# Optimization experiments

Hardware: AMD Instinct MI355X
Metric: run time of the kernel (lower is better)

The kernel has to match this reference:

```python
import jax, jax.numpy as jnp
import numpy as np

N_HEADS = 16
D_MODEL = 1024
HEAD_DIM = D_MODEL // N_HEADS
B, S = 2, 2048


def setup_inputs() -> dict:
    key = jax.random.key(0)
    ks = jax.random.split(key, 10)
    scale = 1.0 / np.sqrt(D_MODEL)
    inp = {
        "query_tokens": jax.random.normal(ks[0], (B, S, D_MODEL), dtype=jnp.float32),
        "key_or_value_tokens": jax.random.normal(ks[1], (B, S, D_MODEL), dtype=jnp.float32),
        "mask": jnp.ones((B, S, S), dtype=jnp.int32),
        "Wq": jax.random.normal(ks[2], (D_MODEL, D_MODEL), dtype=jnp.float32) * scale,
        "bq": jnp.zeros((D_MODEL,), dtype=jnp.float32),
        "Wk": jax.random.normal(ks[3], (D_MODEL, D_MODEL), dtype=jnp.float32) * scale,
        "bk": jnp.zeros((D_MODEL,), dtype=jnp.float32),
        "Wv": jax.random.normal(ks[4], (D_MODEL, D_MODEL), dtype=jnp.float32) * scale,
        "bv": jnp.zeros((D_MODEL,), dtype=jnp.float32),
        "Wo": jax.random.normal(ks[5], (D_MODEL, D_MODEL), dtype=jnp.float32) * scale,
        "bo": jnp.zeros((D_MODEL,), dtype=jnp.float32),
    }
    return inp


def reference(query_tokens, key_or_value_tokens, mask, Wq, bq, Wk, bk, Wv, bv, Wo, bo):
    b, s, d = query_tokens.shape
    h, dh = N_HEADS, HEAD_DIM

    def proj(x, W, bias):
        # torch Linear: x @ W.T + b ; then split heads -> (b, h, s, dh)
        y = jnp.einsum("bsd,ed->bse", x, W) + bias
        return y.reshape(b, -1, h, dh).transpose(0, 2, 1, 3)

    q = proj(query_tokens, Wq, bq)
    k = proj(key_or_value_tokens, Wk, bk)
    v = proj(key_or_value_tokens, Wv, bv)

    scores = jnp.einsum("bhqd,bhkd->bhqk", q, k) / jnp.sqrt(jnp.float32(dh))
    # mask: (b, Sq, Sk) -> (b, 1, Sq, Sk); zeros get large negative fill
    scores = jnp.where(mask[:, None, :, :] == 0, jnp.float32(-1e9), scores)
    attn = jax.nn.softmax(scores, axis=-1)
    out = jnp.einsum("bhqk,bhkd->bhqd", attn, v)
    out = out.transpose(0, 2, 1, 3).reshape(b, s, d)
    return jnp.einsum("bsd,ed->bse", out, Wo) + bo
```

## Files before the change

kernel.cpp:

```cpp
#include <hip/hip_runtime.h>
#include <hip/hip_bf16.h>

typedef __bf16 bf16_8  __attribute__((ext_vector_type(8)));
typedef __bf16 bf16_4  __attribute__((ext_vector_type(4)));
typedef float  f32_4   __attribute__((ext_vector_type(4)));

#define NH 16
#define DHD 64
#define BB 2
#define SS 2048
#define DD 1024

__device__ __forceinline__ void gload16(const __bf16* g, __bf16* l) {
    __builtin_amdgcn_global_load_lds(
        (const __attribute__((address_space(1))) void*)g,
        (__attribute__((address_space(3))) void*)l, 16, 0, 0);
}

__global__ __launch_bounds__(256) void conv_all(
    const float* __restrict__ s0, const float* __restrict__ s1,
    const float* __restrict__ s2, const float* __restrict__ s3,
    const float* __restrict__ s4, const float* __restrict__ s5,
    __bf16* __restrict__ d0, __bf16* __restrict__ d1, __bf16* __restrict__ d2,
    __bf16* __restrict__ d3, __bf16* __restrict__ d4, __bf16* __restrict__ d5) {
    const int y = blockIdx.y;
    if (y >= 2 && blockIdx.x >= 1024) return;
    const float* s = (y == 0) ? s0 : (y == 1) ? s1 : (y == 2) ? s2
                   : (y == 3) ? s3 : (y == 4) ? s4 : s5;
    __bf16* d      = (y == 0) ? d0 : (y == 1) ? d1 : (y == 2) ? d2
                   : (y == 3) ? d3 : (y == 4) ? d4 : d5;
    const int i = (blockIdx.x * 256 + threadIdx.x) * 4;
    f32_4 v = *(const f32_4*)&s[i];
    bf16_4 o; o[0] = (__bf16)v[0]; o[1] = (__bf16)v[1];
    o[2] = (__bf16)v[2]; o[3] = (__bf16)v[3];
    *(bf16_4*)&d[i] = o;
}

__global__ __launch_bounds__(256) void mask_flags_k(const int* __restrict__ mask,
                                                    int* __restrict__ flags) {
    const int id = blockIdx.x;
    const int b = id >> 10, qt = (id >> 5) & 31, kt = id & 31;
    const int t = threadIdx.x;
    const int row = t >> 2, seg = t & 3;
    const int* p = mask + ((size_t)b * SS + qt * 64 + row) * SS + kt * 64 + seg * 16;
    int any0 = 0;
#pragma unroll
    for (int i = 0; i < 4; ++i) {
        int4 v = *(const int4*)&p[i * 4];
        any0 |= (v.x == 0) | (v.y == 0) | (v.z == 0) | (v.w == 0);
    }
    unsigned long long bal = __ballot(any0);
    __shared__ int sf[4];
    if ((t & 63) == 0) sf[t >> 6] = (bal != 0ULL);
    __syncthreads();
    if (t == 0) flags[id] = sf[0] | sf[1] | sf[2] | sf[3];
}

template <int LAYOUT>
__device__ __forceinline__ void gemm_body(const __bf16* __restrict__ A,
                                          const __bf16* __restrict__ W,
                                          const float* __restrict__ bias,
                                          __bf16* __restrict__ out,
                                          __bf16* ldsA, __bf16* ldsB) {
    const int tid  = threadIdx.x;
    const int lane = tid & 63;
    const int w    = tid >> 6;
    const int quad = lane >> 4;
    const int l15  = lane & 15;
    const int wm   = (w >> 1) * 64;
    const int wn   = (w & 1) * 64;
    const int m0   = blockIdx.x * 128;
    const int n0   = blockIdx.y * 128;

    f32_4 acc[4][4] = {};

    for (int kt = 0; kt < 1024; kt += 32) {
#pragma unroll
        for (int cc = 0; cc < 2; ++cc) {
            const int c   = tid + cc * 256;
            const int row = c >> 2;
            const int cp  = c & 3;
            gload16(&A[(size_t)(m0 + row) * 1024 + kt + cp * 8], &ldsA[c * 8]);
            gload16(&W[(size_t)(n0 + row) * 1024 + kt + cp * 8], &ldsB[c * 8]);
        }
        __syncthreads();

        bf16_8 af[4], bfr[4];
#pragma unroll
        for (int i = 0; i < 4; ++i)
            af[i] = *(const bf16_8*)&ldsA[(wm + i * 16 + l15) * 32 + quad * 8];
#pragma unroll
        for (int j = 0; j < 4; ++j)
            bfr[j] = *(const bf16_8*)&ldsB[(wn + j * 16 + l15) * 32 + quad * 8];
#pragma unroll
        for (int i = 0; i < 4; ++i)
#pragma unroll
            for (int j = 0; j < 4; ++j)
                acc[i][j] = __builtin_amdgcn_mfma_f32_16x16x32_bf16(
                    af[i], bfr[j], acc[i][j], 0, 0, 0);
        __syncthreads();
    }

#pragma unroll
    for (int i = 0; i < 4; ++i) {
#pragma unroll
        for (int j = 0; j < 4; ++j) {
            const int col = n0 + wn + j * 16 + l15;
            const float bv = bias[col];
            if (LAYOUT == 2) {
                const int row0 = m0 + wm + i * 16 + quad * 4;
                bf16_4 pk;
#pragma unroll
                for (int r = 0; r < 4; ++r) pk[r] = (__bf16)(acc[i][j][r] + bv);
                const int bb = row0 >> 11, s0 = row0 & 2047;
                const int h = col >> 6, dh = col & 63;
                *(bf16_4*)&out[(((size_t)bb * NH + h) * DHD + dh) * SS + s0] = pk;
            } else {
#pragma unroll
                for (int r = 0; r < 4; ++r) {
                    const int row = m0 + wm + i * 16 + quad * 4 + r;
                    out[(((size_t)(row >> 11) * NH + (col >> 6)) * SS +
                         (row & 2047)) * DHD + (col & 63)] =
                        (__bf16)(acc[i][j][r] + bv);
                }
            }
        }
    }
}

__global__ __launch_bounds__(256) void gemm_qkv(
    const __bf16* __restrict__ Xq, const __bf16* __restrict__ Xkv,
    const __bf16* __restrict__ Wq, const float* __restrict__ bq,
    const __bf16* __restrict__ Wk, const float* __restrict__ bk,
    const __bf16* __restrict__ Wv, const float* __restrict__ bv,
    __bf16* __restrict__ Qo, __bf16* __restrict__ Ko, __bf16* __restrict__ VTo) {
    __shared__ __align__(16) __bf16 ldsA[128 * 32];
    __shared__ __align__(16) __bf16 ldsB[128 * 32];
    const int z = blockIdx.z;
    const __bf16* A    = (z == 0) ? Xq : Xkv;
    const __bf16* W    = (z == 0) ? Wq : (z == 1 ? Wk : Wv);
    const float* bias  = (z == 0) ? bq : (z == 1 ? bk : bv);
    if (z == 2)
        gemm_body<2>(A, W, bias, VTo, ldsA, ldsB);
    else
        gemm_body<0>(A, W, bias, (z == 0) ? Qo : Ko, ldsA, ldsB);
}

__global__ __launch_bounds__(256) void gemm_final(
    const __bf16* __restrict__ A, const __bf16* __restrict__ W,
    const float* __restrict__ bias, float* __restrict__ out) {
    __shared__ __align__(16) __bf16 ldsA[128 * 32];
    __shared__ __align__(16) __bf16 ldsB[64 * 32];
    const int tid  = threadIdx.x;
    const int lane = tid & 63;
    const int w    = tid >> 6;
    const int quad = lane >> 4;
    const int l15  = lane & 15;
    const int wm   = w * 32;
    const int m0   = blockIdx.x * 128;
    const int n0   = blockIdx.y * 64;

    f32_4 acc[2][4] = {};

    for (int kt = 0; kt < 1024; kt += 32) {
#pragma unroll
        for (int cc = 0; cc < 2; ++cc) {
            const int c   = tid + cc * 256;
            const int row = c >> 2;
            const int cp  = c & 3;
            gload16(&A[(size_t)(m0 + row) * 1024 + kt + cp * 8], &ldsA[c * 8]);
        }
        {
            const int c   = tid;
            const int row = c >> 2;
            const int cp  = c & 3;
            gload16(&W[(size_t)(n0 + row) * 1024 + kt + cp * 8], &ldsB[c * 8]);
        }
        __syncthreads();

        bf16_8 af[2], bfr[4];
#pragma unroll
        for (int i = 0; i < 2; ++i)
            af[i] = *(const bf16_8*)&ldsA[(wm + i * 16 + l15) * 32 + quad * 8];
#pragma unroll
        for (int j = 0; j < 4; ++j)
            bfr[j] = *(const bf16_8*)&ldsB[(j * 16 + l15) * 32 + quad * 8];
#pragma unroll
        for (int i = 0; i < 2; ++i)
#pragma unroll
            for (int j = 0; j < 4; ++j)
                acc[i][j] = __builtin_amdgcn_mfma_f32_16x16x32_bf16(
                    af[i], bfr[j], acc[i][j], 0, 0, 0);
        __syncthreads();
    }

#pragma unroll
    for (int i = 0; i < 2; ++i)
#pragma unroll
        for (int j = 0; j < 4; ++j) {
            const int col = n0 + j * 16 + l15;
            const float bv = bias[col];
#pragma unroll
            for (int r = 0; r < 4; ++r) {
                const int row = m0 + wm + i * 16 + quad * 4 + r;
                out[(size_t)row * 1024 + col] = acc[i][j][r] + bv;
            }
        }
}

__global__ __launch_bounds__(512, 4) void flash_attn(
    const __bf16* __restrict__ Q, const __bf16* __restrict__ K,
    const __bf16* __restrict__ VT, const int* __restrict__ mask,
    const int* __restrict__ flags, __bf16* __restrict__ O) {
    __shared__ __align__(16) __bf16 ldsK[64 * 72];
    __shared__ __align__(16) __bf16 ldsVT[64 * 72];
    __shared__ __align__(16) __bf16 ldsP[128 * 72];

    const int tid  = threadIdx.x;
    const int lane = tid & 63;
    const int w    = tid >> 6;
    const int quad = lane >> 4;
    const int l15  = lane & 15;
    const int q0   = blockIdx.x * 128;
    const int bh   = blockIdx.y;
    const int b    = bh >> 4;

    const __bf16* Qb  = Q + (size_t)bh * SS * DHD;
    const __bf16* Kb  = K + (size_t)bh * SS * DHD;
    const __bf16* VTb = VT + (size_t)bh * DHD * SS;
    const int*    mb  = mask + (size_t)b * SS * SS;
    const int*    flb = flags + (size_t)b * 1024 + blockIdx.x * 64;

    bf16_8 qa[2];
#pragma unroll
    for (int ks = 0; ks < 2; ++ks) {
        bf16_8 t = *(const bf16_8*)&Qb[(size_t)(q0 + w * 16 + l15) * DHD +
                                       ks * 32 + quad * 8];
#pragma unroll
        for (int e = 0; e < 8; ++e)
            qa[ks][e] = (__bf16)((float)t[e] * 0.18033688011112042f);
    }

    f32_4 of[4] = {};
    float li[4] = {};

    const int r0 = tid >> 3;
    const int cp = tid & 7;
    uint4 kr = *(const uint4*)&Kb[(size_t)r0 * DHD + cp * 8];
    uint4 vr = *(const uint4*)&VTb[(size_t)r0 * SS + cp * 8];

    for (int k0 = 0; k0 < SS; k0 += 64) {
        *(uint4*)&ldsK[r0 * 72 + cp * 8]  = kr;
        *(uint4*)&ldsVT[r0 * 72 + cp * 8] = vr;
        if (k0 + 64 < SS) {
            const int kn = k0 + 64;
            kr = *(const uint4*)&Kb[(size_t)(kn + r0) * DHD + cp * 8];
            vr = *(const uint4*)&VTb[(size_t)r0 * SS + kn + cp * 8];
        }
        __syncthreads();

        const bool msk = ((flb[k0 >> 6] | flb[32 + (k0 >> 6)]) != 0);

        f32_4 sa[4] = {};
#pragma unroll
        for (int ks = 0; ks < 2; ++ks) {
            bf16_8 kb[4];
#pragma unroll
            for (int j = 0; j < 4; ++j)
                kb[j] = *(const bf16_8*)&ldsK[(j * 16 + l15) * 72 + ks * 32 + quad * 8];
#pragma unroll
            for (int j = 0; j < 4; ++j)
                sa[j] = __builtin_amdgcn_mfma_f32_16x16x32_bf16(
                    qa[ks], kb[j], sa[j], 0, 0, 0);
        }

        if (msk) {
#pragma unroll
            for (int j = 0; j < 4; ++j)
#pragma unroll
                for (int r = 0; r < 4; ++r) {
                    const int qg = q0 + w * 16 + quad * 4 + r;
                    const int kg = k0 + j * 16 + l15;
                    if (mb[(size_t)qg * SS + kg] == 0) sa[j][r] = -1e9f;
                }
        }

#pragma unroll
        for (int j = 0; j < 4; ++j)
#pragma unroll
            for (int r = 0; r < 4; ++r) {
                const float p = exp2f(sa[j][r]);
                li[r] += p;
                ldsP[(w * 16 + quad * 4 + r) * 72 + j * 16 + l15] = (__bf16)p;
            }
        __syncthreads();

#pragma unroll
        for (int ks2 = 0; ks2 < 2; ++ks2) {
            bf16_8 pa, vb[4];
            pa = *(const bf16_8*)&ldsP[(w * 16 + l15) * 72 + ks2 * 32 + quad * 8];
#pragma unroll
            for (int jo = 0; jo < 4; ++jo)
                vb[jo] = *(const bf16_8*)&ldsVT[(jo * 16 + l15) * 72 +
                                                ks2 * 32 + quad * 8];
#pragma unroll
            for (int jo = 0; jo < 4; ++jo)
                of[jo] = __builtin_amdgcn_mfma_f32_16x16x32_bf16(
                    pa, vb[jo], of[jo], 0, 0, 0);
        }
        __syncthreads();
    }

    const int hcol = (bh & 15) * 64;
#pragma unroll
    for (int r = 0; r < 4; ++r) {
        float ls = li[r];
        ls += __shfl_xor(ls, 1);
        ls += __shfl_xor(ls, 2);
        ls += __shfl_xor(ls, 4);
        ls += __shfl_xor(ls, 8);
        const float inv = 1.0f / fmaxf(ls, 1e-37f);
        const int qg = q0 + w * 16 + quad * 4 + r;
#pragma unroll
        for (int jo = 0; jo < 4; ++jo)
            O[((size_t)b * SS + qg) * DD + hcol + jo * 16 + l15] =
                (__bf16)(of[jo][r] * inv);
    }
}


extern "C" void kernel_launch(void* const* d_in, const int* in_sizes, int n_in,
                              void* d_out, int out_size, void* d_ws, size_t ws_size,
                              hipStream_t stream) {
    const float* xq   = (const float*)d_in[0];
    const float* xkv  = (const float*)d_in[1];
    const int*   mask = (const int*)d_in[2];
    const float* Wq   = (const float*)d_in[3];
    const float* bq   = (const float*)d_in[4];
    const float* Wk   = (const float*)d_in[5];
    const float* bk   = (const float*)d_in[6];
    const float* Wv   = (const float*)d_in[7];
    const float* bv   = (const float*)d_in[8];
    const float* Wo   = (const float*)d_in[9];
    const float* bo   = (const float*)d_in[10];

    __bf16* ws = (__bf16*)d_ws;
    const size_t big = (size_t)BB * SS * DD;
    const size_t wsz = (size_t)DD * DD;
    __bf16* Qw   = ws;
    __bf16* Kw   = Qw + big;
    __bf16* VTw  = Kw + big;
    __bf16* Aw   = VTw + big;
    __bf16* Xqb  = Aw + big;
    __bf16* Xkvb = Xqb + big;
    __bf16* Wqb  = Xkvb + big;
    __bf16* Wkb  = Wqb + wsz;
    __bf16* Wvb  = Wkb + wsz;
    __bf16* Wob  = Wvb + wsz;
    int* flags   = (int*)(Wob + wsz);

    conv_all<<<dim3(4096, 6), dim3(256), 0, stream>>>(xq, xkv, Wq, Wk, Wv, Wo,
                                                      Xqb, Xkvb, Wqb, Wkb, Wvb, Wob);
    mask_flags_k<<<dim3(2048), dim3(256), 0, stream>>>(mask, flags);
    gemm_qkv<<<dim3(32, 8, 3), dim3(256), 0, stream>>>(Xqb, Xkvb, Wqb, bq, Wkb, bk,
                                                       Wvb, bv, Qw, Kw, VTw);
    flash_attn<<<dim3(SS / 128, BB * NH), dim3(512), 0, stream>>>(Qw, Kw, VTw, mask,
                                                                  flags, Aw);
    gemm_final<<<dim3(32, 16), dim3(256), 0, stream>>>(Aw, Wob, bo, (float*)d_out);
}
```

Baseline: 274.6 us.

## Restructure flash attention with double-buffered direct-to-LDS loads and 4 waves

The attention kernel moves from 8 waves with 16 query rows each to 4 waves with 32 query rows each, so every K/V fragment read from LDS feeds twice as many MFMAs. K and V^T tiles are now double-buffered in LDS with global_load_lds using an XOR swizzle instead of padding. The QK^T MFMA operands are swapped so each lane holds one query row, which lets P be written as packed 4-element stores, and the barrier between writing and reading P is replaced by an lgkmcnt wait, since each wave only reads back its own rows. The risks are higher register pressure from the doubled accumulators, and fewer waves to hide latency.

```diff
diff --git a/kernel.cpp b/kernel.cpp
--- a/kernel.cpp
+++ b/kernel.cpp
@@ -208,12 +208,12 @@
         }
 }
 
-__global__ __launch_bounds__(512, 4) void flash_attn(
+__global__ __launch_bounds__(256, 2) void flash_attn(
     const __bf16* __restrict__ Q, const __bf16* __restrict__ K,
     const __bf16* __restrict__ VT, const int* __restrict__ mask,
     const int* __restrict__ flags, __bf16* __restrict__ O) {
-    __shared__ __align__(16) __bf16 ldsK[64 * 72];
-    __shared__ __align__(16) __bf16 ldsVT[64 * 72];
+    __shared__ __align__(16) __bf16 ldsK[2][64 * 64];
+    __shared__ __align__(16) __bf16 ldsVT[2][64 * 64];
     __shared__ __align__(16) __bf16 ldsP[128 * 72];
 
     const int tid  = threadIdx.x;
@@ -231,101 +231,133 @@
     const int*    mb  = mask + (size_t)b * SS * SS;
     const int*    flb = flags + (size_t)b * 1024 + blockIdx.x * 64;
 
-    bf16_8 qa[2];
-#pragma unroll
-    for (int ks = 0; ks < 2; ++ks) {
-        bf16_8 t = *(const bf16_8*)&Qb[(size_t)(q0 + w * 16 + l15) * DHD +
-                                       ks * 32 + quad * 8];
-#pragma unroll
-        for (int e = 0; e < 8; ++e)
-            qa[ks][e] = (__bf16)((float)t[e] * 0.18033688011112042f);
-    }
-
-    f32_4 of[4] = {};
-    float li[4] = {};
-
-    const int r0 = tid >> 3;
-    const int cp = tid & 7;
-    uint4 kr = *(const uint4*)&Kb[(size_t)r0 * DHD + cp * 8];
-    uint4 vr = *(const uint4*)&VTb[(size_t)r0 * SS + cp * 8];
+    bf16_8 qa[2][2];
+#pragma unroll
+    for (int mt = 0; mt < 2; ++mt)
+#pragma unroll
+        for (int ks = 0; ks < 2; ++ks) {
+            bf16_8 t = *(const bf16_8*)&Qb[(size_t)(q0 + w * 32 + mt * 16 + l15) * DHD +
+                                           ks * 32 + quad * 8];
+#pragma unroll
+            for (int e = 0; e < 8; ++e)
+                qa[mt][ks][e] = (__bf16)((float)t[e] * 0.18033688011112042f);
+        }
+
+    f32_4 of[2][4] = {};
+    float li[2] = {0.f, 0.f};
+
+    const int c0 = tid, c1 = tid + 256;
+    const int r_0 = c0 >> 3, r_1 = c1 >> 3;
+    const int s_0 = (c0 & 7) ^ (r_0 & 7);
+    const int s_1 = (c1 & 7) ^ (r_1 & 7);
+
+#define STAGE(K0, BUF)                                                         \
+    do {                                                                       \
+        __bf16* lk_ = &ldsK[BUF][0];                                           \
+        __bf16* lv_ = &ldsVT[BUF][0];                                          \
+        gload16(&Kb[(size_t)((K0) + r_0) * DHD + s_0 * 8], &lk_[c0 * 8]);      \
+        gload16(&Kb[(size_t)((K0) + r_1) * DHD + s_1 * 8], &lk_[c1 * 8]);      \
+        gload16(&VTb[(size_t)r_0 * SS + (K0) + s_0 * 8], &lv_[c0 * 8]);        \
+        gload16(&VTb[(size_t)r_1 * SS + (K0) + s_1 * 8], &lv_[c1 * 8]);        \
+    } while (0)
+
+    STAGE(0, 0);
+    __syncthreads();
+
+    const int xq = l15 & 7;
+    int cur = 0;
 
     for (int k0 = 0; k0 < SS; k0 += 64) {
-        *(uint4*)&ldsK[r0 * 72 + cp * 8]  = kr;
-        *(uint4*)&ldsVT[r0 * 72 + cp * 8] = vr;
-        if (k0 + 64 < SS) {
-            const int kn = k0 + 64;
-            kr = *(const uint4*)&Kb[(size_t)(kn + r0) * DHD + cp * 8];
-            vr = *(const uint4*)&VTb[(size_t)r0 * SS + kn + cp * 8];
-        }
-        __syncthreads();
-
+        if (k0 + 64 < SS) STAGE(k0 + 64, cur ^ 1);
+
+        const __bf16* lk = &ldsK[cur][0];
+        const __bf16* lv = &ldsVT[cur][0];
         const bool msk = ((flb[k0 >> 6] | flb[32 + (k0 >> 6)]) != 0);
 
-        f32_4 sa[4] = {};
+        f32_4 sa[2][4] = {};
 #pragma unroll
         for (int ks = 0; ks < 2; ++ks) {
             bf16_8 kb[4];
 #pragma unroll
             for (int j = 0; j < 4; ++j)
-                kb[j] = *(const bf16_8*)&ldsK[(j * 16 + l15) * 72 + ks * 32 + quad * 8];
-#pragma unroll
-            for (int j = 0; j < 4; ++j)
-                sa[j] = __builtin_amdgcn_mfma_f32_16x16x32_bf16(
-                    qa[ks], kb[j], sa[j], 0, 0, 0);
+                kb[j] = *(const bf16_8*)&lk[(j * 16 + l15) * 64 +
+                                            (((ks * 4 + quad) ^ xq) * 8)];
+#pragma unroll
+            for (int mt = 0; mt < 2; ++mt)
+#pragma unroll
+                for (int j = 0; j < 4; ++j)
+                    sa[mt][j] = __builtin_amdgcn_mfma_f32_16x16x32_bf16(
+                        kb[j], qa[mt][ks], sa[mt][j], 0, 0, 0);
         }
 
         if (msk) {
 #pragma unroll
-            for (int j = 0; j < 4; ++j)
+            for (int mt = 0; mt < 2; ++mt)
+#pragma unroll
+                for (int j = 0; j < 4; ++j)
+#pragma unroll
+                    for (int r = 0; r < 4; ++r) {
+                        const int qg = q0 + w * 32 + mt * 16 + l15;
+                        const int kg = k0 + j * 16 + quad * 4 + r;
+                        if (mb[(size_t)qg * SS + kg] == 0) sa[mt][j][r] = -1e9f;
+                    }
+        }
+
+#pragma unroll
+        for (int mt = 0; mt < 2; ++mt)
+#pragma unroll
+            for (int j = 0; j < 4; ++j) {
+                bf16_4 pk;
 #pragma unroll
                 for (int r = 0; r < 4; ++r) {
-                    const int qg = q0 + w * 16 + quad * 4 + r;
-                    const int kg = k0 + j * 16 + l15;
-                    if (mb[(size_t)qg * SS + kg] == 0) sa[j][r] = -1e9f;
+                    const float p = exp2f(sa[mt][j][r]);
+                    li[mt] += p;
+                    pk[r] = (__bf16)p;
                 }
-        }
-
-#pragma unroll
-        for (int j = 0; j < 4; ++j)
-#pragma unroll
-            for (int r = 0; r < 4; ++r) {
-                const float p = exp2f(sa[j][r]);
-                li[r] += p;
-                ldsP[(w * 16 + quad * 4 + r) * 72 + j * 16 + l15] = (__bf16)p;
+                *(bf16_4*)&ldsP[(w * 32 + mt * 16 + l15) * 72 + j * 16 + quad * 4] = pk;
             }
+        asm volatile("s_waitcnt lgkmcnt(0)" ::: "memory");
+
+#pragma unroll
+        for (int ks2 = 0; ks2 < 2; ++ks2) {
+            bf16_8 pa[2], vb[4];
+#pragma unroll
+            for (int mt = 0; mt < 2; ++mt)
+                pa[mt] = *(const bf16_8*)&ldsP[(w * 32 + mt * 16 + l15) * 72 +
+                                               ks2 * 32 + quad * 8];
+#pragma unroll
+            for (int jo = 0; jo < 4; ++jo)
+                vb[jo] = *(const bf16_8*)&lv[(jo * 16 + l15) * 64 +
+                                             (((ks2 * 4 + quad) ^ xq) * 8)];
+#pragma unroll
+            for (int mt = 0; mt < 2; ++mt)
+#pragma unroll
+                for (int jo = 0; jo < 4; ++jo)
+                    of[mt][jo] = __builtin_amdgcn_mfma_f32_16x16x32_bf16(
+                        pa[mt], vb[jo], of[mt][jo], 0, 0, 0);
+        }
+
         __syncthreads();
-
-#pragma unroll
-        for (int ks2 = 0; ks2 < 2; ++ks2) {
-            bf16_8 pa, vb[4];
-            pa = *(const bf16_8*)&ldsP[(w * 16 + l15) * 72 + ks2 * 32 + quad * 8];
+        cur ^= 1;
+    }
+
+    const int hcol = (bh & 15) * 64;
+#pragma unroll
+    for (int mt = 0; mt < 2; ++mt) {
+        float ls = li[mt];
+        ls += __shfl_xor(ls, 16);
+        ls += __shfl_xor(ls, 32);
+#pragma unroll
+        for (int r = 0; r < 4; ++r) {
+            const float inv = 1.0f / fmaxf(__shfl(ls, quad * 4 + r, 16), 1e-37f);
+            const int qg = q0 + w * 32 + mt * 16 + quad * 4 + r;
 #pragma unroll
             for (int jo = 0; jo < 4; ++jo)
-                vb[jo] = *(const bf16_8*)&ldsVT[(jo * 16 + l15) * 72 +
-                                                ks2 * 32 + quad * 8];
-#pragma unroll
-            for (int jo = 0; jo < 4; ++jo)
-                of[jo] = __builtin_amdgcn_mfma_f32_16x16x32_bf16(
-                    pa, vb[jo], of[jo], 0, 0, 0);
-        }
-        __syncthreads();
-    }
-
-    const int hcol = (bh & 15) * 64;
-#pragma unroll
-    for (int r = 0; r < 4; ++r) {
-        float ls = li[r];
-        ls += __shfl_xor(ls, 1);
-        ls += __shfl_xor(ls, 2);
-        ls += __shfl_xor(ls, 4);
-        ls += __shfl_xor(ls, 8);
-        const float inv = 1.0f / fmaxf(ls, 1e-37f);
-        const int qg = q0 + w * 16 + quad * 4 + r;
-#pragma unroll
-        for (int jo = 0; jo < 4; ++jo)
-            O[((size_t)b * SS + qg) * DD + hcol + jo * 16 + l15] =
-                (__bf16)(of[jo][r] * inv);
-    }
+                O[((size_t)b * SS + qg) * DD + hcol + jo * 16 + l15] =
+                    (__bf16)(of[mt][jo][r] * inv);
+        }
+    }
+#undef STAGE
 }
 
 
@@ -364,7 +396,7 @@
     mask_flags_k<<<dim3(2048), dim3(256), 0, stream>>>(mask, flags);
     gemm_qkv<<<dim3(32, 8, 3), dim3(256), 0, stream>>>(Xqb, Xkvb, Wqb, bq, Wkb, bk,
                                                        Wvb, bv, Qw, Kw, VTw);
-    flash_attn<<<dim3(SS / 128, BB * NH), dim3(512), 0, stream>>>(Qw, Kw, VTw, mask,
+    flash_attn<<<dim3(SS / 128, BB * NH), dim3(256), 0, stream>>>(Qw, Kw, VTw, mask,
                                                                   flags, Aw);
     gemm_final<<<dim3(32, 16), dim3(256), 0, stream>>>(Aw, Wob, bo, (float*)d_out);
 }
```

Result: faster. 262.3 us (-4.5%).
